# Kernel tuning notes

Hardware: AMD Instinct MI355X
Metric: run time of the kernel (lower is better)

## Reference

```python
import jax, jax.numpy as jnp
import numpy as np

QUERY_DIM = 1024
KEY_DIM = 1024
NUM_HEADS = 16
HEAD_DIM = QUERY_DIM // NUM_HEADS


def setup_inputs() -> dict:
    key = jax.random.key(0)
    ks = jax.random.split(key, 11)
    B, Sq, Sk = 2, 2048, 2048
    s = 0.02
    return {
        "q": jax.random.normal(ks[0], (B, Sq, QUERY_DIM), jnp.float32),
        "k": jax.random.normal(ks[1], (B, Sk, KEY_DIM), jnp.float32),
        "v": jax.random.normal(ks[2], (B, Sk, KEY_DIM), jnp.float32),
        "Wq": jax.random.normal(ks[3], (QUERY_DIM, QUERY_DIM), jnp.float32) * s,
        "bq": jnp.zeros((QUERY_DIM,), jnp.float32),
        "Wk": jax.random.normal(ks[4], (KEY_DIM, QUERY_DIM), jnp.float32) * s,
        "bk": jnp.zeros((QUERY_DIM,), jnp.float32),
        "Wv": jax.random.normal(ks[5], (KEY_DIM, QUERY_DIM), jnp.float32) * s,
        "bv": jnp.zeros((QUERY_DIM,), jnp.float32),
        "Wo": jax.random.normal(ks[6], (QUERY_DIM, QUERY_DIM), jnp.float32) * s,
        "bo": jnp.zeros((QUERY_DIM,), jnp.float32),
    }


def reference(q, k, v, Wq, bq, Wk, bk, Wv, bv, Wo, bo):
    B, Sq, _ = q.shape
    Sk = k.shape[1]
    scale = HEAD_DIM ** -0.5
    # projections -> [B, H, S, Dh]
    qh = (q @ Wq + bq).reshape(B, Sq, NUM_HEADS, HEAD_DIM).transpose(0, 2, 1, 3)
    kh = (k @ Wk + bk).reshape(B, Sk, NUM_HEADS, HEAD_DIM).transpose(0, 2, 1, 3)
    vh = (v @ Wv + bv).reshape(B, Sk, NUM_HEADS, HEAD_DIM).transpose(0, 2, 1, 3)
    scores = jnp.einsum("bhqd,bhkd->bhqk", qh, kh) * scale
    attn = jax.nn.softmax(scores, axis=-1)
    out = jnp.einsum("bhqk,bhkd->bhqd", attn, vh)
    out = out.transpose(0, 2, 1, 3).reshape(B, Sq, QUERY_DIM)
    return out @ Wo + bo  # dropout is identity at inference
```

## Files before the change

kernel.cpp:

```cpp
#include <hip/hip_runtime.h>
#include <hip/hip_fp16.h>
#include <cstddef>


#define B_   2
#define S_   2048
#define D_   1024
#define H_   16
#define DH_  64

typedef _Float16 half8 __attribute__((ext_vector_type(8)));
typedef _Float16 half4 __attribute__((ext_vector_type(4)));
typedef _Float16 half2v __attribute__((ext_vector_type(2)));
typedef float floatx4 __attribute__((ext_vector_type(4)));
typedef float floatx16 __attribute__((ext_vector_type(16)));
typedef int intx4 __attribute__((ext_vector_type(4)));

#define MFMA32(a, b, c) __builtin_amdgcn_mfma_f32_16x16x32_f16((a), (b), (c), 0, 0, 0)
#define MFMA3216(a, b, c) __builtin_amdgcn_mfma_f32_32x32x16_f16((a), (b), (c), 0, 0, 0)

#if __has_builtin(__builtin_amdgcn_fdot2)
#define LP_FDOT2 1
#else
#define LP_FDOT2 0
#endif

#define GLD_AS(p) ((const __attribute__((address_space(1))) void*)(p))
#define LDS_AS(p) ((__attribute__((address_space(3))) void*)(p))

__device__ __forceinline__ void half_swap(int& a, int& b, const int hi) {
#if __has_builtin(__builtin_amdgcn_permlane32_swap)
    (void)hi;
    auto r = __builtin_amdgcn_permlane32_swap(a, b, false, false);
    a = r[0]; b = r[1];
#else
    const int ax = __shfl_xor(a, 32, 64), bx = __shfl_xor(b, 32, 64);
    const int na = hi ? bx : a;
    b = hi ? b : ax;
    a = na;
#endif
}

__global__ __launch_bounds__(256) void prep(
    const float* __restrict__ q, const float* __restrict__ k,
    const float* __restrict__ v,
    __half* __restrict__ qf, __half* __restrict__ kf, __half* __restrict__ vf,
    const float* __restrict__ Wq, const float* __restrict__ Wk,
    const float* __restrict__ Wv, const float* __restrict__ Wo,
    __half* __restrict__ Wtq, __half* __restrict__ Wtk,
    __half* __restrict__ Wtv, __half* __restrict__ Wto)
{
    __shared__ __align__(16) __half T[64][72];
    const int tid = threadIdx.x;
    const int z = blockIdx.z;
    if (z < 3) {
        const float* srcs[3] = {q, k, v};
        __half* dsts[3] = {qf, kf, vf};
        const int i = blockIdx.x * 256 + tid;
        const float4* s = (const float4*)srcs[z];
        const float4 a = s[2 * i], b = s[2 * i + 1];
        half8 h;
        h[0] = (_Float16)a.x; h[1] = (_Float16)a.y; h[2] = (_Float16)a.z; h[3] = (_Float16)a.w;
        h[4] = (_Float16)b.x; h[5] = (_Float16)b.y; h[6] = (_Float16)b.z; h[7] = (_Float16)b.w;
        *(half8*)&dsts[z][(size_t)i * 8] = h;
        return;
    }
    if (blockIdx.x >= 256) return;
    const float* Ws[4] = {Wq, Wk, Wv, Wo};
    __half* Wts[4] = {Wtq, Wtk, Wtv, Wto};
    const int n0 = (blockIdx.x & 15) * 64, k0 = (blockIdx.x >> 4) * 64;
    for (int w = 0; w < 4; ++w) {
        const float* W = Ws[w];
        __half* Wt = Wts[w];
        #pragma unroll
        for (int p = 0; p < 4; ++p) {
            const int c = tid + p * 256;
            const int kr = c >> 4, nc = (c & 15) * 4;
            const float4 a = *(const float4*)&W[(size_t)(k0 + kr) * D_ + n0 + nc];
            T[nc + 0][kr] = __float2half(a.x);
            T[nc + 1][kr] = __float2half(a.y);
            T[nc + 2][kr] = __float2half(a.z);
            T[nc + 3][kr] = __float2half(a.w);
        }
        __syncthreads();
        #pragma unroll
        for (int p = 0; p < 2; ++p) {
            const int c = tid + p * 256;
            const int nr = c >> 3, kc = (c & 7) * 8;
            *(half8*)&Wt[(size_t)(n0 + nr) * D_ + k0 + kc] = *(const half8*)&T[nr][kc];
        }
        __syncthreads();
    }
}

__device__ __forceinline__ void gemm_core(
    const __half* __restrict__ A, const __half* __restrict__ Bt,
    const float* __restrict__ bias, void* __restrict__ dst,
    const int mode, const float oscale, const int m0, const int n0)
{
    __shared__ __align__(16) char gsm[34816];
    __half* Asl = (__half*)gsm;
    __half* Bsl = (__half*)(gsm + 16384);

    const int tid = threadIdx.x;
    const int lane = tid & 63, wv = tid >> 6;
    const int quad = lane >> 4, lr = lane & 15;
    const int wm0 = (wv >> 1) * 64, wn0 = (wv & 1) * 64;

    floatx4 acc[4][4];
    #pragma unroll
    for (int i = 0; i < 4; ++i)
        #pragma unroll
        for (int j = 0; j < 4; ++j)
            acc[i][j] = (floatx4){0.f, 0.f, 0.f, 0.f};

    const int rowb = wv * 32 + (lane >> 3);
    const int colb = (lane & 7) * 8;
    const __half* gA = A  + (size_t)(m0 + rowb) * D_ + colb;
    const __half* gB = Bt + (size_t)(n0 + rowb) * D_ + colb;

    for (int k0 = 0; k0 < D_; k0 += 64) {
        __syncthreads();
        #pragma unroll
        for (int p = 0; p < 4; ++p) {
            __builtin_amdgcn_global_load_lds(
                GLD_AS(gA + (size_t)p * 8 * D_),
                LDS_AS(gsm + (wv * 4 + p) * 1024), 16, 0, 0);
            __builtin_amdgcn_global_load_lds(
                GLD_AS(gB + (size_t)p * 8 * D_),
                LDS_AS(gsm + 16384 + (wv * 4 + p) * 1024), 16, 0, 0);
        }
        gA += 64; gB += 64;
        __syncthreads();

        __builtin_amdgcn_s_setprio(1);
        #pragma unroll
        for (int ks = 0; ks < 2; ++ks) {
            const int ko = quad * 8 + ks * 32;
            half8 af[4], bf[4];
            #pragma unroll
            for (int i = 0; i < 4; ++i)
                af[i] = *(const half8*)&Asl[(wm0 + i * 16 + lr) * 64 + ko];
            #pragma unroll
            for (int j = 0; j < 4; ++j)
                bf[j] = *(const half8*)&Bsl[(wn0 + j * 16 + lr) * 64 + ko];
            #pragma unroll
            for (int i = 0; i < 4; ++i)
                #pragma unroll
                for (int j = 0; j < 4; ++j)
                    acc[i][j] = MFMA32(af[i], bf[j], acc[i][j]);
        }
        __builtin_amdgcn_s_setprio(0);
    }

    if (mode == 1) {
        float* out = (float*)dst;
        #pragma unroll
        for (int i = 0; i < 4; ++i) {
            #pragma unroll
            for (int j = 0; j < 4; ++j) {
                const int col = n0 + wn0 + j * 16 + lr;
                const float bval = bias[col];
                #pragma unroll
                for (int r = 0; r < 4; ++r) {
                    const int m = m0 + wm0 + i * 16 + quad * 4 + r;
                    out[(size_t)m * D_ + col] = acc[i][j][r] + bval;
                }
            }
        }
        return;
    }

    __syncthreads();
    __half (*Ct)[136] = (__half(*)[136])gsm;
    #pragma unroll
    for (int i = 0; i < 4; ++i) {
        #pragma unroll
        for (int j = 0; j < 4; ++j) {
            const int nl = wn0 + j * 16 + lr;
            const float bval = bias[n0 + nl];
            #pragma unroll
            for (int r = 0; r < 4; ++r) {
                const int ml = wm0 + i * 16 + quad * 4 + r;
                const _Float16 hv = (_Float16)((acc[i][j][r] + bval) * oscale);
                if (mode == 0) Ct[ml][nl] = hv;
                else           Ct[nl][ml] = hv;
            }
        }
    }
    __syncthreads();
    __half* oh = (__half*)dst;
    #pragma unroll
    for (int p = 0; p < 8; ++p) {
        const int row = (tid >> 4) + p * 16;
        const int cs  = (tid & 15) * 8;
        const half8 vls = *(const half8*)&Ct[row][cs];
        if (mode == 0) {
            const int m = m0 + row, col = n0 + cs;
            const int b = m >> 11, s = m & (S_ - 1);
            const int h = col >> 6, d = col & 63;
            *(half8*)&oh[(((size_t)(b * H_ + h) * S_ + s) << 6) + d] = vls;
        } else {
            const int col = n0 + row, m = m0 + cs;
            const int b = m >> 11, s = m & (S_ - 1);
            const int h = col >> 6, d = col & 63;
            *(half8*)&oh[((size_t)(b * H_ + h) * DH_ + d) * S_ + s] = vls;
        }
    }
}

__global__ __launch_bounds__(256) void gemm_proj(
    const __half* __restrict__ qf, const __half* __restrict__ kf,
    const __half* __restrict__ vf,
    const __half* __restrict__ Wtq, const __half* __restrict__ Wtk,
    const __half* __restrict__ Wtv,
    const float* __restrict__ bq, const float* __restrict__ bk,
    const float* __restrict__ bv,
    __half* __restrict__ qhf, __half* __restrict__ khf, __half* __restrict__ vht)
{
    const int flat = blockIdx.x + (blockIdx.y << 3) + (blockIdx.z << 8);
    const int wid = (flat & 7) * 96 + (flat >> 3);
    const int z = wid >> 8;
    const int rem = wid & 255;
    const int m0 = (rem >> 3) * 128, n0 = (rem & 7) * 128;

    const __half* As[3] = {qf, kf, vf};
    const __half* Bts[3] = {Wtq, Wtk, Wtv};
    const float* bs[3] = {bq, bk, bv};
    __half* ds[3] = {qhf, khf, vht};
    gemm_core(As[z], Bts[z], bs[z], ds[z], z == 2 ? 2 : 0,
              z == 0 ? 0.1803368801111244f : 1.0f, m0, n0);
}

__global__ __launch_bounds__(256) void gemm_final(
    const __half* __restrict__ attf, const __half* __restrict__ Wto,
    const float* __restrict__ bo, float* __restrict__ out)
{
    const int flat = blockIdx.x + (blockIdx.y << 3);
    const int wid = (flat & 7) * 32 + (flat >> 3);
    const int m0 = (wid >> 3) * 128, n0 = (wid & 7) * 128;
    gemm_core(attf, Wto, bo, out, 1, 1.0f, m0, n0);
}

__global__ __launch_bounds__(512, 4) void attn_f16(
    const __half* __restrict__ qhf, const __half* __restrict__ khf,
    const __half* __restrict__ vht, __half* __restrict__ attf)
{
    __shared__ __align__(16) char smem[36864];

    const int tid = threadIdx.x;
    const int lane = tid & 63, wv = tid >> 6;
    const int l31 = lane & 31, hi = lane >> 5;
    const int kb = wv >> 2, qb = wv & 3;
    const int flat = blockIdx.x + (blockIdx.y << 4);
    const int wid = ((flat & 7) << 6) + (flat >> 3);
    const int bh = wid >> 4;
    const int q0 = (wid & 15) * 128;
    const size_t hbase = (size_t)bh * S_ * DH_;

    half8 qB[4];
    #pragma unroll
    for (int ds = 0; ds < 4; ++ds)
        qB[ds] = *(const half8*)&qhf[hbase
            + (size_t)(q0 + qb * 32 + l31) * DH_ + ds * 16 + hi * 8];

    float lp0 = 0.f, lp1 = 0.f;
#if !LP_FDOT2
    float lp2 = 0.f, lp3 = 0.f;
#endif
    floatx16 O[2];
    #pragma unroll
    for (int i = 0; i < 16; ++i) { O[0][i] = 0.f; O[1][i] = 0.f; }

    const int srow = tid >> 3, sseg = (tid & 7) * 8;
    const __half* kg = khf + hbase + (size_t)srow * DH_ + sseg;
    const __half* vg = vht + hbase + (size_t)srow * S_ + sseg;

    {
        __half (*K0)[72] = (__half(*)[72])smem;
        __half (*V0)[72] = (__half(*)[72])(smem + 9216);
        *(half8*)&K0[srow][sseg] = *(const half8*)kg;
        *(half8*)&V0[srow][sseg] = *(const half8*)vg;
    }
    kg += 64 * DH_; vg += 64;
    half8 pk = *(const half8*)kg;
    half8 pv = *(const half8*)vg;
    __syncthreads();

    const half2v one2 = {(_Float16)1.0f, (_Float16)1.0f};

    for (int kt = 0; kt < S_; kt += 64) {
        const int cb = (kt >> 6) & 1;
        __half (*Ks)[72] = (__half(*)[72])(smem + cb * 18432);
        __half (*Vs)[72] = (__half(*)[72])(smem + cb * 18432 + 9216);
        __half (*Kn)[72] = (__half(*)[72])(smem + (cb ^ 1) * 18432);
        __half (*Vn)[72] = (__half(*)[72])(smem + (cb ^ 1) * 18432 + 9216);

        if (kt + 64 < S_) {
            *(half8*)&Kn[srow][sseg] = pk;
            *(half8*)&Vn[srow][sseg] = pv;
            if (kt + 128 < S_) {
                kg += 64 * DH_; vg += 64;
                pk = *(const half8*)kg;
                pv = *(const half8*)vg;
            }
        }

        floatx16 s;
        #pragma unroll
        for (int i = 0; i < 16; ++i) s[i] = 0.f;
        __builtin_amdgcn_s_setprio(1);
        #pragma unroll
        for (int ds = 0; ds < 4; ++ds) {
            const half8 aK = *(const half8*)&Ks[kb * 32 + l31][ds * 16 + hi * 8];
            s = MFMA3216(aK, qB[ds], s);
        }
        __builtin_amdgcn_s_setprio(0);

        #pragma unroll
        for (int r = 0; r < 16; ++r) {
            const float e = __builtin_amdgcn_exp2f(s[r]);
#if !LP_FDOT2
            (r & 2) ? ((r & 1) ? (lp3 += e) : (lp2 += e))
                    : ((r & 1) ? (lp1 += e) : (lp0 += e));
#endif
            s[r] = e;
        }

        half8 pB[2];
        int PW[2][4];
        #pragma unroll
        for (int ks = 0; ks < 2; ++ks) {
            int P0 = __builtin_bit_cast(int, __builtin_amdgcn_cvt_pkrtz(s[ks * 8 + 0], s[ks * 8 + 1]));
            int P1 = __builtin_bit_cast(int, __builtin_amdgcn_cvt_pkrtz(s[ks * 8 + 2], s[ks * 8 + 3]));
            int P2 = __builtin_bit_cast(int, __builtin_amdgcn_cvt_pkrtz(s[ks * 8 + 4], s[ks * 8 + 5]));
            int P3 = __builtin_bit_cast(int, __builtin_amdgcn_cvt_pkrtz(s[ks * 8 + 6], s[ks * 8 + 7]));
            half_swap(P0, P2, hi);
            half_swap(P1, P3, hi);
            PW[ks][0] = P0; PW[ks][1] = P1; PW[ks][2] = P2; PW[ks][3] = P3;
            const intx4 w = {P0, P1, P2, P3};
            pB[ks] = __builtin_bit_cast(half8, w);
        }

        __builtin_amdgcn_s_setprio(1);
        #pragma unroll
        for (int db = 0; db < 2; ++db)
            #pragma unroll
            for (int ks = 0; ks < 2; ++ks) {
                const half8 aV = *(const half8*)&Vs[db * 32 + l31][kb * 32 + ks * 16 + hi * 8];
                O[db] = MFMA3216(aV, pB[ks], O[db]);
            }
        __builtin_amdgcn_s_setprio(0);

#if LP_FDOT2
        #pragma unroll
        for (int ks = 0; ks < 2; ++ks) {
            lp0 = __builtin_amdgcn_fdot2(__builtin_bit_cast(half2v, PW[ks][0]), one2, lp0, false);
            lp1 = __builtin_amdgcn_fdot2(__builtin_bit_cast(half2v, PW[ks][1]), one2, lp1, false);
            lp0 = __builtin_amdgcn_fdot2(__builtin_bit_cast(half2v, PW[ks][2]), one2, lp0, false);
            lp1 = __builtin_amdgcn_fdot2(__builtin_bit_cast(half2v, PW[ks][3]), one2, lp1, false);
        }
#endif

        __syncthreads();
    }

    float (*R)[132] = (float(*)[132])smem;
    float* Lred = (float*)(smem + 33792);

#if LP_FDOT2
    float lp = lp0 + lp1;
#else
    float lp = (lp0 + lp1) + (lp2 + lp3);
#endif
    lp += __shfl_xor(lp, 32, 64);
    const int qg = qb * 32 + l31;
    if (lane < 32) Lred[kb * 128 + qg] = lp;
    if (kb == 1) {
        #pragma unroll
        for (int db = 0; db < 2; ++db)
            #pragma unroll
            for (int r = 0; r < 16; ++r) {
                const int d = db * 32 + (r & 3) + 8 * (r >> 2) + 4 * hi;
                R[d][qg] = O[db][r];
            }
    }
    __syncthreads();
    if (kb == 0) {
        const float il = 1.0f / (Lred[qg] + Lred[128 + qg]);
        #pragma unroll
        for (int db = 0; db < 2; ++db)
            #pragma unroll
            for (int r = 0; r < 16; ++r) {
                const int d = db * 32 + (r & 3) + 8 * (r >> 2) + 4 * hi;
                O[db][r] = (O[db][r] + R[d][qg]) * il;
            }
    }
    __syncthreads();
    __half (*F)[72] = (__half(*)[72])smem;
    if (kb == 0) {
        #pragma unroll
        for (int db = 0; db < 2; ++db)
            #pragma unroll
            for (int t = 0; t < 4; ++t) {
                half4 hv;
                #pragma unroll
                for (int r = 0; r < 4; ++r) hv[r] = (_Float16)O[db][t * 4 + r];
                *(half4*)&F[qg][db * 32 + t * 8 + hi * 4] = hv;
            }
    }
    __syncthreads();

    const int b = bh >> 4, h = bh & 15;
    const int qrow = tid >> 2, dseg = (tid & 3) * 16;
    __half* dstp = &attf[(((size_t)(b * S_ + q0 + qrow)) << 10) + h * DH_ + dseg];
    *(half8*)&dstp[0] = *(const half8*)&F[qrow][dseg];
    *(half8*)&dstp[8] = *(const half8*)&F[qrow][dseg + 8];
}

extern "C" void kernel_launch(void* const* d_in, const int* in_sizes, int n_in,
                              void* d_out, int out_size, void* d_ws, size_t ws_size,
                              hipStream_t stream) {
    const float* q  = (const float*)d_in[0];
    const float* k  = (const float*)d_in[1];
    const float* v  = (const float*)d_in[2];
    const float* Wq = (const float*)d_in[3];
    const float* bq = (const float*)d_in[4];
    const float* Wk = (const float*)d_in[5];
    const float* bk = (const float*)d_in[6];
    const float* Wv = (const float*)d_in[7];
    const float* bv = (const float*)d_in[8];
    const float* Wo = (const float*)d_in[9];
    const float* bo = (const float*)d_in[10];
    float* out = (float*)d_out;

    __half* ws = (__half*)d_ws;
    const size_t NE = (size_t)B_ * S_ * D_;
    __half* qf   = ws;
    __half* kf   = ws + NE;
    __half* vf   = ws + 2 * NE;
    __half* qhf  = ws + 3 * NE;
    __half* khf  = ws + 4 * NE;
    __half* vht  = ws + 5 * NE;
    __half* attf = ws + 6 * NE;
    __half* Wtq  = ws + 7 * NE;
    __half* Wtk  = Wtq + (size_t)D_ * D_;
    __half* Wtv  = Wtk + (size_t)D_ * D_;
    __half* Wto  = Wtv + (size_t)D_ * D_;

    const dim3 blk(256);
    prep<<<dim3((unsigned)(NE / 8 / 256), 1, 4), blk, 0, stream>>>(
        q, k, v, qf, kf, vf, Wq, Wk, Wv, Wo, Wtq, Wtk, Wtv, Wto);

    gemm_proj<<<dim3(D_ / 128, (B_ * S_) / 128, 3), blk, 0, stream>>>(
        qf, kf, vf, Wtq, Wtk, Wtv, bq, bk, bv, qhf, khf, vht);

    attn_f16<<<dim3(S_ / 128, B_ * H_), dim3(512), 0, stream>>>(qhf, khf, vht, attf);

    gemm_final<<<dim3(D_ / 128, (B_ * S_) / 128), blk, 0, stream>>>(attf, Wto, bo, out);
}
```

Measured before the change: 222.4 us.

## Load K/V MFMA operands directly from global memory instead of shared-memory staging

The attention kernel no longer stages K and V tiles in double-buffered LDS with a per-iteration barrier. Each wave now loads its MFMA operand fragments straight from global memory into registers and drops the __syncthreads in the inner loop. This removes the LDS writes and reads and the block-wide synchronisation. In exchange, each K/V element is fetched once per q-block wave instead of once per block, so more traffic goes through the L1/L2 caches, and the loads are issued inside the loop with no software prefetch ahead of the dependent MFMAs.

```diff
diff --git a/kernel.cpp b/kernel.cpp
--- a/kernel.cpp
+++ b/kernel.cpp
@@ -246,7 +246,7 @@
     const __half* __restrict__ qhf, const __half* __restrict__ khf,
     const __half* __restrict__ vht, __half* __restrict__ attf)
 {
-    __shared__ __align__(16) char smem[36864];
+    __shared__ __align__(16) char smem[34816];
 
     const int tid = threadIdx.x;
     const int lane = tid & 63, wv = tid >> 6;
@@ -272,49 +272,31 @@
     #pragma unroll
     for (int i = 0; i < 16; ++i) { O[0][i] = 0.f; O[1][i] = 0.f; }
 
-    const int srow = tid >> 3, sseg = (tid & 7) * 8;
-    const __half* kg = khf + hbase + (size_t)srow * DH_ + sseg;
-    const __half* vg = vht + hbase + (size_t)srow * S_ + sseg;
-
-    {
-        __half (*K0)[72] = (__half(*)[72])smem;
-        __half (*V0)[72] = (__half(*)[72])(smem + 9216);
-        *(half8*)&K0[srow][sseg] = *(const half8*)kg;
-        *(half8*)&V0[srow][sseg] = *(const half8*)vg;
-    }
-    kg += 64 * DH_; vg += 64;
-    half8 pk = *(const half8*)kg;
-    half8 pv = *(const half8*)vg;
-    __syncthreads();
+    const __half* kp = khf + hbase + (size_t)(kb * 32 + l31) * DH_ + hi * 8;
+    const __half* vp = vht + hbase + (size_t)l31 * S_ + kb * 32 + hi * 8;
 
     const half2v one2 = {(_Float16)1.0f, (_Float16)1.0f};
 
     for (int kt = 0; kt < S_; kt += 64) {
-        const int cb = (kt >> 6) & 1;
-        __half (*Ks)[72] = (__half(*)[72])(smem + cb * 18432);
-        __half (*Vs)[72] = (__half(*)[72])(smem + cb * 18432 + 9216);
-        __half (*Kn)[72] = (__half(*)[72])(smem + (cb ^ 1) * 18432);
-        __half (*Vn)[72] = (__half(*)[72])(smem + (cb ^ 1) * 18432 + 9216);
-
-        if (kt + 64 < S_) {
-            *(half8*)&Kn[srow][sseg] = pk;
-            *(half8*)&Vn[srow][sseg] = pv;
-            if (kt + 128 < S_) {
-                kg += 64 * DH_; vg += 64;
-                pk = *(const half8*)kg;
-                pv = *(const half8*)vg;
-            }
-        }
+        half8 kA[4], vA[4];
+        #pragma unroll
+        for (int ds = 0; ds < 4; ++ds)
+            kA[ds] = *(const half8*)(kp + ds * 16);
+        #pragma unroll
+        for (int db = 0; db < 2; ++db)
+            #pragma unroll
+            for (int ks = 0; ks < 2; ++ks)
+                vA[db * 2 + ks] = *(const half8*)(vp + (size_t)db * 32 * S_ + ks * 16);
+        kp += 64 * DH_;
+        vp += 64;
 
         floatx16 s;
         #pragma unroll
         for (int i = 0; i < 16; ++i) s[i] = 0.f;
         __builtin_amdgcn_s_setprio(1);
         #pragma unroll
-        for (int ds = 0; ds < 4; ++ds) {
-            const half8 aK = *(const half8*)&Ks[kb * 32 + l31][ds * 16 + hi * 8];
-            s = MFMA3216(aK, qB[ds], s);
-        }
+        for (int ds = 0; ds < 4; ++ds)
+            s = MFMA3216(kA[ds], qB[ds], s);
         __builtin_amdgcn_s_setprio(0);
 
         #pragma unroll
@@ -346,10 +328,8 @@
         #pragma unroll
         for (int db = 0; db < 2; ++db)
             #pragma unroll
-            for (int ks = 0; ks < 2; ++ks) {
-                const half8 aV = *(const half8*)&Vs[db * 32 + l31][kb * 32 + ks * 16 + hi * 8];
-                O[db] = MFMA3216(aV, pB[ks], O[db]);
-            }
+            for (int ks = 0; ks < 2; ++ks)
+                O[db] = MFMA3216(vA[db * 2 + ks], pB[ks], O[db]);
         __builtin_amdgcn_s_setprio(0);
 
 #if LP_FDOT2
@@ -361,8 +341,6 @@
             lp1 = __builtin_amdgcn_fdot2(__builtin_bit_cast(half2v, PW[ks][3]), one2, lp1, false);
         }
 #endif
-
-        __syncthreads();
     }
 
     float (*R)[132] = (float(*)[132])smem;
```

Measured after the change: 299.1 us. +34.5%, slower.

## Widen attention block to 1024 threads with four-way key split

Applied to the files above, without the earlier changes.

The attention kernel now runs 16 waves per block. Four key-groups each process 32 keys of a 128-key tile, and their partial outputs are reduced through shared memory at the end. The double-buffered K/V shared tiles become a single buffer holding 128 keys, with two syncthreads per iteration instead of one. This trades the load/compute overlap and the launch bound of 4 blocks per CU for more in-block parallelism and fewer loop iterations. It also adds a longer serial reduction in the epilogue.

```diff
diff --git a/kernel.cpp b/kernel.cpp
--- a/kernel.cpp
+++ b/kernel.cpp
@@ -242,11 +242,14 @@
     gemm_core(attf, Wto, bo, out, 1, 1.0f, m0, n0);
 }
 
-__global__ __launch_bounds__(512, 4) void attn_f16(
+__global__ __launch_bounds__(1024) void attn_f16(
     const __half* __restrict__ qhf, const __half* __restrict__ khf,
     const __half* __restrict__ vht, __half* __restrict__ attf)
 {
     __shared__ __align__(16) char smem[36864];
+    __half (*Ks)[72] = (__half(*)[72])smem;
+    __half (*V0)[72] = (__half(*)[72])(smem + 18432);
+    __half (*V1)[72] = (__half(*)[72])(smem + 27648);
 
     const int tid = threadIdx.x;
     const int lane = tid & 63, wv = tid >> 6;
@@ -272,39 +275,28 @@
     #pragma unroll
     for (int i = 0; i < 16; ++i) { O[0][i] = 0.f; O[1][i] = 0.f; }
 
-    const int srow = tid >> 3, sseg = (tid & 7) * 8;
-    const __half* kg = khf + hbase + (size_t)srow * DH_ + sseg;
-    const __half* vg = vht + hbase + (size_t)srow * S_ + sseg;
-
-    {
-        __half (*K0)[72] = (__half(*)[72])smem;
-        __half (*V0)[72] = (__half(*)[72])(smem + 9216);
-        *(half8*)&K0[srow][sseg] = *(const half8*)kg;
-        *(half8*)&V0[srow][sseg] = *(const half8*)vg;
-    }
-    kg += 64 * DH_; vg += 64;
+    const int krow = tid >> 3, kseg = (tid & 7) * 8;
+    const int vrow = tid >> 4, vcol = (tid & 15) * 8;
+    __half* vdst = (vcol < 64) ? &V0[vrow][vcol] : &V1[vrow][vcol - 64];
+    const __half* kg = khf + hbase + (size_t)krow * DH_ + kseg;
+    const __half* vg = vht + hbase + (size_t)vrow * S_ + vcol;
+
     half8 pk = *(const half8*)kg;
     half8 pv = *(const half8*)vg;
-    __syncthreads();
 
     const half2v one2 = {(_Float16)1.0f, (_Float16)1.0f};
-
-    for (int kt = 0; kt < S_; kt += 64) {
-        const int cb = (kt >> 6) & 1;
-        __half (*Ks)[72] = (__half(*)[72])(smem + cb * 18432);
-        __half (*Vs)[72] = (__half(*)[72])(smem + cb * 18432 + 9216);
-        __half (*Kn)[72] = (__half(*)[72])(smem + (cb ^ 1) * 18432);
-        __half (*Vn)[72] = (__half(*)[72])(smem + (cb ^ 1) * 18432 + 9216);
-
-        if (kt + 64 < S_) {
-            *(half8*)&Kn[srow][sseg] = pk;
-            *(half8*)&Vn[srow][sseg] = pv;
-            if (kt + 128 < S_) {
-                kg += 64 * DH_; vg += 64;
-                pk = *(const half8*)kg;
-                pv = *(const half8*)vg;
-            }
-        }
+    const int vband = (kb & 1) * 32;
+
+    for (int kt = 0; kt < S_; kt += 128) {
+        __syncthreads();
+        *(half8*)&Ks[krow][kseg] = pk;
+        *(half8*)vdst = pv;
+        if (kt + 128 < S_) {
+            kg += 128 * DH_; vg += 128;
+            pk = *(const half8*)kg;
+            pv = *(const half8*)vg;
+        }
+        __syncthreads();
 
         floatx16 s;
         #pragma unroll
@@ -342,12 +334,13 @@
             pB[ks] = __builtin_bit_cast(half8, w);
         }
 
+        __half (*Vsub)[72] = (kb < 2) ? V0 : V1;
         __builtin_amdgcn_s_setprio(1);
         #pragma unroll
         for (int db = 0; db < 2; ++db)
             #pragma unroll
             for (int ks = 0; ks < 2; ++ks) {
-                const half8 aV = *(const half8*)&Vs[db * 32 + l31][kb * 32 + ks * 16 + hi * 8];
+                const half8 aV = *(const half8*)&Vsub[db * 32 + l31][vband + ks * 16 + hi * 8];
                 O[db] = MFMA3216(aV, pB[ks], O[db]);
             }
         __builtin_amdgcn_s_setprio(0);
@@ -361,12 +354,11 @@
             lp1 = __builtin_amdgcn_fdot2(__builtin_bit_cast(half2v, PW[ks][3]), one2, lp1, false);
         }
 #endif
-
-        __syncthreads();
-    }
-
-    float (*R)[132] = (float(*)[132])smem;
-    float* Lred = (float*)(smem + 33792);
+    }
+
+    __syncthreads();
+    float (*R)[68] = (float(*)[68])smem;
+    float* Lred = (float*)(smem + 34816);
 
 #if LP_FDOT2
     float lp = lp0 + lp1;
@@ -376,46 +368,53 @@
     lp += __shfl_xor(lp, 32, 64);
     const int qg = qb * 32 + l31;
     if (lane < 32) Lred[kb * 128 + qg] = lp;
-    if (kb == 1) {
-        #pragma unroll
-        for (int db = 0; db < 2; ++db)
-            #pragma unroll
-            for (int r = 0; r < 16; ++r) {
-                const int d = db * 32 + (r & 3) + 8 * (r >> 2) + 4 * hi;
-                R[d][qg] = O[db][r];
-            }
-    }
-    __syncthreads();
-    if (kb == 0) {
-        const float il = 1.0f / (Lred[qg] + Lred[128 + qg]);
-        #pragma unroll
-        for (int db = 0; db < 2; ++db)
-            #pragma unroll
-            for (int r = 0; r < 16; ++r) {
-                const int d = db * 32 + (r & 3) + 8 * (r >> 2) + 4 * hi;
-                O[db][r] = (O[db][r] + R[d][qg]) * il;
-            }
-    }
-    __syncthreads();
+
+    #pragma unroll
+    for (int r = 1; r < 4; ++r) {
+        if (kb == r) {
+            #pragma unroll
+            for (int db = 0; db < 2; ++db)
+                #pragma unroll
+                for (int t = 0; t < 4; ++t) {
+                    const floatx4 v4 = {O[db][t * 4 + 0], O[db][t * 4 + 1],
+                                        O[db][t * 4 + 2], O[db][t * 4 + 3]};
+                    *(floatx4*)&R[qg][db * 32 + t * 8 + hi * 4] = v4;
+                }
+        }
+        __syncthreads();
+        if (kb == 0) {
+            #pragma unroll
+            for (int db = 0; db < 2; ++db)
+                #pragma unroll
+                for (int t = 0; t < 4; ++t) {
+                    const floatx4 v4 = *(const floatx4*)&R[qg][db * 32 + t * 8 + hi * 4];
+                    #pragma unroll
+                    for (int j = 0; j < 4; ++j) O[db][t * 4 + j] += v4[j];
+                }
+        }
+        __syncthreads();
+    }
+
     __half (*F)[72] = (__half(*)[72])smem;
     if (kb == 0) {
+        const float il = 1.0f / (Lred[qg] + Lred[128 + qg]
+                               + Lred[256 + qg] + Lred[384 + qg]);
         #pragma unroll
         for (int db = 0; db < 2; ++db)
             #pragma unroll
             for (int t = 0; t < 4; ++t) {
                 half4 hv;
                 #pragma unroll
-                for (int r = 0; r < 4; ++r) hv[r] = (_Float16)O[db][t * 4 + r];
+                for (int j = 0; j < 4; ++j) hv[j] = (_Float16)(O[db][t * 4 + j] * il);
                 *(half4*)&F[qg][db * 32 + t * 8 + hi * 4] = hv;
             }
     }
     __syncthreads();
 
     const int b = bh >> 4, h = bh & 15;
-    const int qrow = tid >> 2, dseg = (tid & 3) * 16;
-    __half* dstp = &attf[(((size_t)(b * S_ + q0 + qrow)) << 10) + h * DH_ + dseg];
-    *(half8*)&dstp[0] = *(const half8*)&F[qrow][dseg];
-    *(half8*)&dstp[8] = *(const half8*)&F[qrow][dseg + 8];
+    const int qrow = tid >> 3, dseg = (tid & 7) * 8;
+    *(half8*)&attf[(((size_t)(b * S_ + q0 + qrow)) << 10) + h * DH_ + dseg]
+        = *(const half8*)&F[qrow][dseg];
 }
 
 extern "C" void kernel_launch(void* const* d_in, const int* in_sizes, int n_in,
@@ -455,7 +454,7 @@
     gemm_proj<<<dim3(D_ / 128, (B_ * S_) / 128, 3), blk, 0, stream>>>(
         qf, kf, vf, Wtq, Wtk, Wtv, bq, bk, bv, qhf, khf, vht);
 
-    attn_f16<<<dim3(S_ / 128, B_ * H_), dim3(512), 0, stream>>>(qhf, khf, vht, attf);
+    attn_f16<<<dim3(S_ / 128, B_ * H_), dim3(1024), 0, stream>>>(qhf, khf, vht, attf);
 
     gemm_final<<<dim3(D_ / 128, (B_ * S_) / 128), blk, 0, stream>>>(attf, Wto, bo, out);
 }
```

Result: no change. 224.0 us (+0.7%).

## Fuse fp32-to-fp16 input conversion into projection GEMM A-tile loads

Applied to the files above, without the earlier changes.

Removes the separate q/k/v fp32-to-fp16 conversion pass. The projection GEMM now reads fp32 activations directly into registers, converts them and stores them to LDS, prefetching the next k-slice while the current one is computed. The weight transpose becomes its own kernel with one block per 64x64 tile per weight matrix, giving 1024 blocks instead of 256 blocks that each looped over four weights. This saves a full write and re-read of three fp16 activation tensors. The cost is twice the global bytes per A tile across 8 N-tiles, which re-read the fp32 input, plus extra register pressure and synchronous conversion in the GEMM loop.

```diff
diff --git a/kernel.cpp b/kernel.cpp
--- a/kernel.cpp
+++ b/kernel.cpp
@@ -41,60 +41,42 @@
 #endif
 }
 
-__global__ __launch_bounds__(256) void prep(
-    const float* __restrict__ q, const float* __restrict__ k,
-    const float* __restrict__ v,
-    __half* __restrict__ qf, __half* __restrict__ kf, __half* __restrict__ vf,
+__global__ __launch_bounds__(256) void wtrans4(
     const float* __restrict__ Wq, const float* __restrict__ Wk,
     const float* __restrict__ Wv, const float* __restrict__ Wo,
     __half* __restrict__ Wtq, __half* __restrict__ Wtk,
     __half* __restrict__ Wtv, __half* __restrict__ Wto)
 {
     __shared__ __align__(16) __half T[64][72];
-    const int tid = threadIdx.x;
-    const int z = blockIdx.z;
-    if (z < 3) {
-        const float* srcs[3] = {q, k, v};
-        __half* dsts[3] = {qf, kf, vf};
-        const int i = blockIdx.x * 256 + tid;
-        const float4* s = (const float4*)srcs[z];
-        const float4 a = s[2 * i], b = s[2 * i + 1];
-        half8 h;
-        h[0] = (_Float16)a.x; h[1] = (_Float16)a.y; h[2] = (_Float16)a.z; h[3] = (_Float16)a.w;
-        h[4] = (_Float16)b.x; h[5] = (_Float16)b.y; h[6] = (_Float16)b.z; h[7] = (_Float16)b.w;
-        *(half8*)&dsts[z][(size_t)i * 8] = h;
-        return;
-    }
-    if (blockIdx.x >= 256) return;
     const float* Ws[4] = {Wq, Wk, Wv, Wo};
     __half* Wts[4] = {Wtq, Wtk, Wtv, Wto};
-    const int n0 = (blockIdx.x & 15) * 64, k0 = (blockIdx.x >> 4) * 64;
-    for (int w = 0; w < 4; ++w) {
-        const float* W = Ws[w];
-        __half* Wt = Wts[w];
-        #pragma unroll
-        for (int p = 0; p < 4; ++p) {
-            const int c = tid + p * 256;
-            const int kr = c >> 4, nc = (c & 15) * 4;
-            const float4 a = *(const float4*)&W[(size_t)(k0 + kr) * D_ + n0 + nc];
-            T[nc + 0][kr] = __float2half(a.x);
-            T[nc + 1][kr] = __float2half(a.y);
-            T[nc + 2][kr] = __float2half(a.z);
-            T[nc + 3][kr] = __float2half(a.w);
-        }
-        __syncthreads();
-        #pragma unroll
-        for (int p = 0; p < 2; ++p) {
-            const int c = tid + p * 256;
-            const int nr = c >> 3, kc = (c & 7) * 8;
-            *(half8*)&Wt[(size_t)(n0 + nr) * D_ + k0 + kc] = *(const half8*)&T[nr][kc];
-        }
-        __syncthreads();
-    }
-}
-
+    const float* W = Ws[blockIdx.z];
+    __half* Wt = Wts[blockIdx.z];
+    const int tid = threadIdx.x;
+    const int n0 = blockIdx.x * 64, k0 = blockIdx.y * 64;
+    #pragma unroll
+    for (int p = 0; p < 4; ++p) {
+        const int c = tid + p * 256;
+        const int kr = c >> 4, nc = (c & 15) * 4;
+        const float4 a = *(const float4*)&W[(size_t)(k0 + kr) * D_ + n0 + nc];
+        T[nc + 0][kr] = __float2half(a.x);
+        T[nc + 1][kr] = __float2half(a.y);
+        T[nc + 2][kr] = __float2half(a.z);
+        T[nc + 3][kr] = __float2half(a.w);
+    }
+    __syncthreads();
+    #pragma unroll
+    for (int p = 0; p < 2; ++p) {
+        const int c = tid + p * 256;
+        const int nr = c >> 3, kc = (c & 7) * 8;
+        *(half8*)&Wt[(size_t)(n0 + nr) * D_ + k0 + kc] = *(const half8*)&T[nr][kc];
+    }
+}
+
+template<int AF32>
 __device__ __forceinline__ void gemm_core(
-    const __half* __restrict__ A, const __half* __restrict__ Bt,
+    const __half* __restrict__ A, const float* __restrict__ A32,
+    const __half* __restrict__ Bt,
     const float* __restrict__ bias, void* __restrict__ dst,
     const int mode, const float oscale, const int m0, const int n0)
 {
@@ -119,18 +101,54 @@
     const __half* gA = A  + (size_t)(m0 + rowb) * D_ + colb;
     const __half* gB = Bt + (size_t)(n0 + rowb) * D_ + colb;
 
+    float4 pa32[4][2];
+    if (AF32) {
+        #pragma unroll
+        for (int p = 0; p < 4; ++p) {
+            const int c = tid + p * 256;
+            const float* src = A32 + (size_t)(m0 + (c >> 3)) * D_ + (c & 7) * 8;
+            pa32[p][0] = *(const float4*)src;
+            pa32[p][1] = *(const float4*)(src + 4);
+        }
+    }
+
     for (int k0 = 0; k0 < D_; k0 += 64) {
         __syncthreads();
-        #pragma unroll
-        for (int p = 0; p < 4; ++p) {
-            __builtin_amdgcn_global_load_lds(
-                GLD_AS(gA + (size_t)p * 8 * D_),
-                LDS_AS(gsm + (wv * 4 + p) * 1024), 16, 0, 0);
+        if (AF32) {
+            #pragma unroll
+            for (int p = 0; p < 4; ++p) {
+                const int c = tid + p * 256;
+                half8 h;
+                h[0] = (_Float16)pa32[p][0].x; h[1] = (_Float16)pa32[p][0].y;
+                h[2] = (_Float16)pa32[p][0].z; h[3] = (_Float16)pa32[p][0].w;
+                h[4] = (_Float16)pa32[p][1].x; h[5] = (_Float16)pa32[p][1].y;
+                h[6] = (_Float16)pa32[p][1].z; h[7] = (_Float16)pa32[p][1].w;
+                *(half8*)&Asl[(c >> 3) * 64 + (c & 7) * 8] = h;
+            }
+        } else {
+            #pragma unroll
+            for (int p = 0; p < 4; ++p)
+                __builtin_amdgcn_global_load_lds(
+                    GLD_AS(gA + (size_t)p * 8 * D_),
+                    LDS_AS(gsm + (wv * 4 + p) * 1024), 16, 0, 0);
+            gA += 64;
+        }
+        #pragma unroll
+        for (int p = 0; p < 4; ++p)
             __builtin_amdgcn_global_load_lds(
                 GLD_AS(gB + (size_t)p * 8 * D_),
                 LDS_AS(gsm + 16384 + (wv * 4 + p) * 1024), 16, 0, 0);
-        }
-        gA += 64; gB += 64;
+        gB += 64;
+        if (AF32 && k0 + 64 < D_) {
+            #pragma unroll
+            for (int p = 0; p < 4; ++p) {
+                const int c = tid + p * 256;
+                const float* src = A32 + (size_t)(m0 + (c >> 3)) * D_
+                                       + k0 + 64 + (c & 7) * 8;
+                pa32[p][0] = *(const float4*)src;
+                pa32[p][1] = *(const float4*)(src + 4);
+            }
+        }
         __syncthreads();
 
         __builtin_amdgcn_s_setprio(1);
@@ -210,8 +228,8 @@
 }
 
 __global__ __launch_bounds__(256) void gemm_proj(
-    const __half* __restrict__ qf, const __half* __restrict__ kf,
-    const __half* __restrict__ vf,
+    const float* __restrict__ q, const float* __restrict__ k,
+    const float* __restrict__ v,
     const __half* __restrict__ Wtq, const __half* __restrict__ Wtk,
     const __half* __restrict__ Wtv,
     const float* __restrict__ bq, const float* __restrict__ bk,
@@ -224,12 +242,12 @@
     const int rem = wid & 255;
     const int m0 = (rem >> 3) * 128, n0 = (rem & 7) * 128;
 
-    const __half* As[3] = {qf, kf, vf};
+    const float* As32[3] = {q, k, v};
     const __half* Bts[3] = {Wtq, Wtk, Wtv};
     const float* bs[3] = {bq, bk, bv};
     __half* ds[3] = {qhf, khf, vht};
-    gemm_core(As[z], Bts[z], bs[z], ds[z], z == 2 ? 2 : 0,
-              z == 0 ? 0.1803368801111244f : 1.0f, m0, n0);
+    gemm_core<1>(nullptr, As32[z], Bts[z], bs[z], ds[z], z == 2 ? 2 : 0,
+                 z == 0 ? 0.1803368801111244f : 1.0f, m0, n0);
 }
 
 __global__ __launch_bounds__(256) void gemm_final(
@@ -239,7 +257,7 @@
     const int flat = blockIdx.x + (blockIdx.y << 3);
     const int wid = (flat & 7) * 32 + (flat >> 3);
     const int m0 = (wid >> 3) * 128, n0 = (wid & 7) * 128;
-    gemm_core(attf, Wto, bo, out, 1, 1.0f, m0, n0);
+    gemm_core<0>(attf, nullptr, Wto, bo, out, 1, 1.0f, m0, n0);
 }
 
 __global__ __launch_bounds__(512, 4) void attn_f16(
@@ -436,9 +454,6 @@
 
     __half* ws = (__half*)d_ws;
     const size_t NE = (size_t)B_ * S_ * D_;
-    __half* qf   = ws;
-    __half* kf   = ws + NE;
-    __half* vf   = ws + 2 * NE;
     __half* qhf  = ws + 3 * NE;
     __half* khf  = ws + 4 * NE;
     __half* vht  = ws + 5 * NE;
@@ -449,11 +464,10 @@
     __half* Wto  = Wtv + (size_t)D_ * D_;
 
     const dim3 blk(256);
-    prep<<<dim3((unsigned)(NE / 8 / 256), 1, 4), blk, 0, stream>>>(
-        q, k, v, qf, kf, vf, Wq, Wk, Wv, Wo, Wtq, Wtk, Wtv, Wto);
+    wtrans4<<<dim3(16, 16, 4), blk, 0, stream>>>(Wq, Wk, Wv, Wo, Wtq, Wtk, Wtv, Wto);
 
     gemm_proj<<<dim3(D_ / 128, (B_ * S_) / 128, 3), blk, 0, stream>>>(
-        qf, kf, vf, Wtq, Wtk, Wtv, bq, bk, bv, qhf, khf, vht);
+        q, k, v, Wtq, Wtk, Wtv, bq, bk, bv, qhf, khf, vht);
 
     attn_f16<<<dim3(S_ / 128, B_ * H_), dim3(512), 0, stream>>>(qhf, khf, vht, attf);
 
```

Result: slower. 237.7 us (+6.9%).
